# Kernel optimization log

Measured on AMD Instinct MI355X. Metric: run time of the kernel, lower is better.

## Reference

```python
import jax, jax.numpy as jnp
import numpy as np

D_MODEL = 1024
N_HEADS = 16
D_HEAD = D_MODEL // N_HEADS


def setup_inputs() -> dict:
    key = jax.random.key(0)
    ks = jax.random.split(key, 5)
    scale = 1.0 / np.sqrt(D_MODEL)
    return {
        "x": jax.random.normal(ks[0], (2, 2048, D_MODEL), dtype=jnp.float32),
        "W_q": jax.random.normal(ks[1], (D_MODEL, D_MODEL), dtype=jnp.float32) * scale,
        "W_k": jax.random.normal(ks[2], (D_MODEL, D_MODEL), dtype=jnp.float32) * scale,
        "W_v": jax.random.normal(ks[3], (D_MODEL, D_MODEL), dtype=jnp.float32) * scale,
        "W_o": jax.random.normal(ks[4], (D_MODEL, D_MODEL), dtype=jnp.float32) * scale,
    }


def reference(x, W_q, W_k, W_v, W_o):
    B, S, _ = x.shape
    # nn.Linear computes x @ W.T; weights stored [out, in]
    def proj(W):
        y = jnp.einsum("bsd,ed->bse", x, W)
        return y.reshape(B, S, N_HEADS, D_HEAD).transpose(0, 2, 1, 3)  # [B,H,S,Dh]

    q, k, v = proj(W_q), proj(W_k), proj(W_v)
    scores = jnp.einsum("bhqd,bhkd->bhqk", q, k) / jnp.sqrt(jnp.float32(D_HEAD))
    causal = jnp.triu(jnp.ones((S, S), dtype=bool), k=1)
    scores = jnp.where(causal, -jnp.inf, scores)
    attn = jax.nn.softmax(scores, axis=-1)
    out = jnp.einsum("bhqk,bhkd->bhqd", attn, v)  # [B,H,S,Dh]
    out = out.transpose(0, 2, 1, 3).reshape(B, S, D_MODEL)
    return jnp.einsum("bsd,ed->bse", out, W_o)
```

## Files before the change

### kernel.cpp

```cpp
#include <hip/hip_runtime.h>


#define DMODEL 1024
#define NHEADS 16
#define DHEAD  64
#define SEQ    2048
#define BATCH  2
#define MROWS  (BATCH * SEQ)

typedef __bf16 bf16x8 __attribute__((ext_vector_type(8)));
typedef __bf16 bf16x4 __attribute__((ext_vector_type(4)));
typedef float  f32x4  __attribute__((ext_vector_type(4)));

__device__ __forceinline__ f32x4 mfma16(bf16x8 a, bf16x8 b, f32x4 c) {
    return __builtin_amdgcn_mfma_f32_16x16x32_bf16(a, b, c, 0, 0, 0);
}

template <int N>
__device__ __forceinline__ void waitcnt_vm() {
    asm volatile("s_waitcnt vmcnt(%0)" :: "i"(N) : "memory");
}

__device__ __forceinline__ bf16x8 ld8(const float* p) {
    const f32x4 a0 = *(const f32x4*)p;
    const f32x4 a1 = *(const f32x4*)(p + 4);
    bf16x8 v;
    v[0] = (__bf16)a0[0]; v[1] = (__bf16)a0[1];
    v[2] = (__bf16)a0[2]; v[3] = (__bf16)a0[3];
    v[4] = (__bf16)a1[0]; v[5] = (__bf16)a1[1];
    v[6] = (__bf16)a1[2]; v[7] = (__bf16)a1[3];
    return v;
}

__device__ __forceinline__ void gll16(const __bf16* g, __bf16* l) {
    __builtin_amdgcn_global_load_lds(
        (const __attribute__((address_space(1))) void*)g,
        (__attribute__((address_space(3))) void*)l,
        16, 0, 0);
}

__global__ __launch_bounds__(256) void cvt_kernel(const float* __restrict__ x,
                                                  const float* __restrict__ Wq,
                                                  const float* __restrict__ Wk,
                                                  const float* __restrict__ Wv,
                                                  const float* __restrict__ Wo,
                                                  __bf16* __restrict__ xb,
                                                  __bf16* __restrict__ wcat) {
    const int c = blockIdx.x * 256 + threadIdx.x;
    if (c < 524288) {
        *(bf16x8*)(xb + (size_t)c * 8) = ld8(x + (size_t)c * 8);
    } else {
        const int i = c - 524288;
        const int w = i >> 17;
        const int j = i & 131071;
        const float* src = (w == 0) ? Wq : (w == 1) ? Wk : (w == 2) ? Wv : Wo;
        *(bf16x8*)(wcat + (size_t)w * DMODEL * DMODEL + (size_t)j * 8) =
            ld8(src + (size_t)j * 8);
    }
}

template <typename TC, int MREP, int NREP>
__device__ __forceinline__ void gemm_bb_body(const __bf16* __restrict__ A,
                                             const __bf16* __restrict__ W,
                                             TC* __restrict__ C,
                                             __bf16* __restrict__ VT,
                                             bool vt, int m0, int bn0, int cn0,
                                             float scale) {
    constexpr int K  = DMODEL;
    constexpr int TM = MREP * 32;
    constexpr int TN = NREP * 32;
    constexpr int L  = MREP / 2 + NREP / 2;
    __shared__ __align__(16) __bf16 As[3][TM][32];
    __shared__ __align__(16) __bf16 Bs[3][TN][32];

    const int tid  = threadIdx.x;
    const int lane = tid & 63;
    const int wave = tid >> 6;
    const int quad = lane >> 4;
    const int l16  = lane & 15;
    const int wm   = wave & 1;
    const int wn   = wave >> 1;

    const int srow = lane >> 2;
    const int scol = (lane & 3) * 8;

    const __bf16* ap = A + (size_t)(m0 + srow) * K + scol;
    const __bf16* bp = W + (size_t)(bn0 + srow) * K + scol;

    f32x4 acc[MREP][NREP] = {};

    auto stage = [&](int kn, int buf) {
#pragma unroll
        for (int j = 0; j < MREP / 2; ++j) {
            const int r = wave * (MREP * 8) + j * 16;
            gll16(ap + (size_t)r * K + kn, &As[buf][r][0]);
        }
#pragma unroll
        for (int j = 0; j < NREP / 2; ++j) {
            const int r = wave * (NREP * 8) + j * 16;
            gll16(bp + (size_t)r * K + kn, &Bs[buf][r][0]);
        }
    };

    stage(0, 0);
    stage(32, 1);

    int cur = 0;
    for (int k0 = 0; k0 < K; k0 += 32) {
        if (k0 + 64 < K) {
            int b2 = cur + 2; if (b2 >= 3) b2 -= 3;
            stage(k0 + 64, b2);
            waitcnt_vm<2 * L>();
        } else if (k0 + 32 < K) {
            waitcnt_vm<L>();
        } else {
            waitcnt_vm<0>();
        }
        __builtin_amdgcn_s_barrier();
        __builtin_amdgcn_sched_barrier(0);

        bf16x8 af[MREP], bfr[NREP];
#pragma unroll
        for (int i = 0; i < MREP; ++i)
            af[i] = *(const bf16x8*)(&As[cur][wm * (MREP * 16) + i * 16 + l16][quad * 8]);
#pragma unroll
        for (int j = 0; j < NREP; ++j)
            bfr[j] = *(const bf16x8*)(&Bs[cur][wn * (NREP * 16) + j * 16 + l16][quad * 8]);
#pragma unroll
        for (int mi = 0; mi < MREP; ++mi)
#pragma unroll
            for (int ni = 0; ni < NREP; ++ni)
                acc[mi][ni] = mfma16(af[mi], bfr[ni], acc[mi][ni]);

        __builtin_amdgcn_sched_barrier(0);
        __builtin_amdgcn_s_barrier();
        int c1 = cur + 1; if (c1 >= 3) c1 -= 3;
        cur = c1;
    }

    if (!vt) {
#pragma unroll
        for (int mi = 0; mi < MREP; ++mi)
#pragma unroll
            for (int ni = 0; ni < NREP; ++ni)
#pragma unroll
                for (int r = 0; r < 4; ++r) {
                    int row = m0 + wm * (MREP * 16) + mi * 16 + quad * 4 + r;
                    int col = cn0 + wn * (NREP * 16) + ni * 16 + l16;
                    C[(size_t)row * DMODEL + col] = (TC)(acc[mi][ni][r] * scale);
                }
    } else {
#pragma unroll
        for (int mi = 0; mi < MREP; ++mi)
#pragma unroll
            for (int ni = 0; ni < NREP; ++ni) {
                const int m  = m0 + wm * (MREP * 16) + mi * 16 + quad * 4;
                const int hd = cn0 + wn * (NREP * 16) + ni * 16 + l16;
                bf16x4 v4;
#pragma unroll
                for (int r = 0; r < 4; ++r) v4[r] = (__bf16)acc[mi][ni][r];
                *(bf16x4*)(VT + (size_t)hd * MROWS + m) = v4;
            }
    }
}

#define QSCALE 0.1803368801111204f

__global__ __launch_bounds__(256) void qkv_kernel(const __bf16* __restrict__ X,
                                                  const __bf16* __restrict__ wcat,
                                                  __bf16* __restrict__ Q,
                                                  __bf16* __restrict__ K,
                                                  __bf16* __restrict__ VT) {
    const int bn0 = blockIdx.x * 128;
    const int z   = bn0 >> 10;
    const int cn0 = bn0 - (z << 10);
    __bf16* Y = (z == 0) ? Q : K;
    const float scale = (z == 0) ? QSCALE : 1.0f;
    gemm_bb_body<__bf16, 4, 4>(X, wcat, Y, VT, z == 2,
                               blockIdx.y * 128, bn0, cn0, scale);
}

__global__ __launch_bounds__(256) void out_gemm_kernel(const __bf16* __restrict__ A,
                                                       const __bf16* __restrict__ W,
                                                       float* __restrict__ C) {
    gemm_bb_body<float, 2, 4>(A, W, C, nullptr, false,
                              blockIdx.y * 64, blockIdx.x * 128, blockIdx.x * 128,
                              1.0f);
}

__global__ __launch_bounds__(256) void attn_kernel(const __bf16* __restrict__ Q,
                                                   const __bf16* __restrict__ Kg,
                                                   const __bf16* __restrict__ VTg,
                                                   __bf16* __restrict__ O) {
    const int bh  = blockIdx.x;
    const int y   = blockIdx.y;
    const int ya  = y >> 3, yr = y & 7;
    const int qt2 = (ya == 0) ? (31 - yr)
                  : (ya == 1) ? (16 + yr)
                  : (ya == 2) ? (15 - yr)
                  :             yr;
    const int b = bh >> 4, h = bh & 15;
    const size_t base = (size_t)b * SEQ * DMODEL + (size_t)h * DHEAD;

    const int tid  = threadIdx.x;
    const int lane = tid & 63;
    const int wave = tid >> 6;
    const int quad = lane >> 4;
    const int l16  = lane & 15;

    __shared__ __align__(16) __bf16 Ks[2][64][64];
    __shared__ __align__(16) __bf16 Vs[2][64][64];
    __shared__ __align__(16) __bf16 Ps[4][2][16][40];

    const int sr = lane >> 3;
    const int sc = ((lane & 7) ^ sr) * 8;

    const int qrow = qt2 * 64 + wave * 16 + l16;

    const bf16x8 qf0 = *(const bf16x8*)(Q + base + (size_t)qrow * DMODEL + quad * 8);
    const bf16x8 qf1 = *(const bf16x8*)(Q + base + (size_t)qrow * DMODEL + 32 + quad * 8);

    const __bf16* kp = Kg + base + (size_t)(wave * 16 + sr) * DMODEL + sc;
    const __bf16* vp = VTg + (size_t)(h * 64 + wave * 16 + sr) * MROWS
                           + (size_t)b * SEQ + sc;

    bf16x8 ones;
#pragma unroll
    for (int i = 0; i < 8; ++i) ones[i] = (__bf16)1.0f;

    f32x4 oacc[4] = {};
    f32x4 lacc = {};

    const int ntiles = qt2 + 1;
    const int gsw = (l16 & 7);

    gll16(kp, &Ks[0][wave * 16][0]);
    gll16(kp + (size_t)8 * DMODEL, &Ks[0][wave * 16 + 8][0]);
    gll16(vp, &Vs[0][wave * 16][0]);
    gll16(vp + (size_t)8 * MROWS, &Vs[0][wave * 16 + 8][0]);
    __syncthreads();

    int cur = 0;
    for (int kt = 0; kt < ntiles; ++kt) {
        const int k0 = kt * 64;

        if (kt + 1 < ntiles) {
            const __bf16* kpt = kp + (size_t)(k0 + 64) * DMODEL;
            const __bf16* vpt = vp + (k0 + 64);
            gll16(kpt, &Ks[cur ^ 1][wave * 16][0]);
            gll16(kpt + (size_t)8 * DMODEL, &Ks[cur ^ 1][wave * 16 + 8][0]);
            gll16(vpt, &Vs[cur ^ 1][wave * 16][0]);
            gll16(vpt + (size_t)8 * MROWS, &Vs[cur ^ 1][wave * 16 + 8][0]);
        }

        const bool diag = (kt == ntiles - 1);

        f32x4 s[4];
#pragma unroll
        for (int g = 0; g < 4; ++g) {
            const bf16x8 kfa = *(const bf16x8*)(&Ks[cur][g * 16 + l16][(quad ^ gsw) * 8]);
            const bf16x8 kfb = *(const bf16x8*)(&Ks[cur][g * 16 + l16][((quad + 4) ^ gsw) * 8]);
            f32x4 t = {};
            t = mfma16(kfa, qf0, t);
            t = mfma16(kfb, qf1, t);
            s[g] = t;
        }

        bf16x4 w4[4];
        if (!diag) {
#pragma unroll
            for (int g = 0; g < 4; ++g)
#pragma unroll
                for (int r = 0; r < 4; ++r)
                    w4[g][r] = (__bf16)exp2f(s[g][r]);
        } else {
#pragma unroll
            for (int g = 0; g < 4; ++g)
#pragma unroll
                for (int r = 0; r < 4; ++r) {
                    const int kk = k0 + g * 16 + quad * 4 + r;
                    w4[g][r] = (kk <= qrow) ? (__bf16)exp2f(s[g][r]) : (__bf16)0.f;
                }
        }

#pragma unroll
        for (int g = 0; g < 4; ++g)
            *(bf16x4*)(&Ps[wave][g >> 1][l16][(g & 1) * 16 + quad * 4]) = w4[g];

        const bf16x8 pf0 = *(const bf16x8*)(&Ps[wave][0][l16][quad * 8]);
        const bf16x8 pf1 = *(const bf16x8*)(&Ps[wave][1][l16][quad * 8]);
        lacc = mfma16(ones, pf0, lacc);
        lacc = mfma16(ones, pf1, lacc);
#pragma unroll
        for (int f = 0; f < 4; ++f) {
            const bf16x8 vfa = *(const bf16x8*)(&Vs[cur][f * 16 + l16][(quad ^ gsw) * 8]);
            const bf16x8 vfb = *(const bf16x8*)(&Vs[cur][f * 16 + l16][((quad + 4) ^ gsw) * 8]);
            f32x4 t = oacc[f];
            t = mfma16(vfa, pf0, t);
            t = mfma16(vfb, pf1, t);
            oacc[f] = t;
        }

        __syncthreads();
        cur ^= 1;
    }

    const float l_i = lacc[0];
    const float inv = (l_i > 0.f) ? (1.f / l_i) : 0.f;
#pragma unroll
    for (int f = 0; f < 4; ++f) {
        bf16x4 o;
#pragma unroll
        for (int r = 0; r < 4; ++r) o[r] = (__bf16)(oacc[f][r] * inv);
        *(bf16x4*)(O + base + (size_t)qrow * DMODEL + f * 16 + quad * 4) = o;
    }
}

extern "C" void kernel_launch(void* const* d_in, const int* in_sizes, int n_in,
                              void* d_out, int out_size, void* d_ws, size_t ws_size,
                              hipStream_t stream) {
    const float* x  = (const float*)d_in[0];
    const float* Wq = (const float*)d_in[1];
    const float* Wk = (const float*)d_in[2];
    const float* Wv = (const float*)d_in[3];
    const float* Wo = (const float*)d_in[4];
    float* out = (float*)d_out;

    const size_t tm = (size_t)MROWS * DMODEL;
    const size_t tw = (size_t)DMODEL * DMODEL;
    __bf16* Q    = (__bf16*)d_ws;
    __bf16* K    = Q + tm;
    __bf16* VT   = K + tm;
    __bf16* xb   = VT + tm;
    __bf16* wcat = xb + tm;

    cvt_kernel<<<4096, 256, 0, stream>>>(x, Wq, Wk, Wv, Wo, xb, wcat);

    dim3 g1(3072 / 128, MROWS / 128);
    qkv_kernel<<<g1, 256, 0, stream>>>(xb, wcat, Q, K, VT);

    dim3 g2(BATCH * NHEADS, SEQ / 64);
    attn_kernel<<<g2, 256, 0, stream>>>(Q, K, VT, Q);

    dim3 g3(DMODEL / 128, MROWS / 64);
    out_gemm_kernel<<<g3, 256, 0, stream>>>(Q, wcat + 3 * tw, out);
}
```

Before: 177.6 us.

## Process two query tiles per attention block and swap P via permlane

Each attention workgroup now handles 128 query rows (two 64-row tiles A and B) instead of 64. Every K/V tile loaded into shared memory is therefore reused for twice as many queries, which halves K/V global traffic and the number of blocks. The P matrix is also moved from the softmax layout to the MFMA operand layout with v_permlane32/16_swap register shuffles instead of a round trip through shared memory. The cost is higher register pressure from two sets of accumulators, fewer blocks (512 instead of 1024), and wasted masked work on tile A's final diagonal iteration.

```diff
diff --git a/kernel.cpp b/kernel.cpp
--- a/kernel.cpp
+++ b/kernel.cpp
@@ -192,13 +192,9 @@
                                                    const __bf16* __restrict__ Kg,
                                                    const __bf16* __restrict__ VTg,
                                                    __bf16* __restrict__ O) {
-    const int bh  = blockIdx.x;
-    const int y   = blockIdx.y;
-    const int ya  = y >> 3, yr = y & 7;
-    const int qt2 = (ya == 0) ? (31 - yr)
-                  : (ya == 1) ? (16 + yr)
-                  : (ya == 2) ? (15 - yr)
-                  :             yr;
+    const int bh = blockIdx.x;
+    const int y  = blockIdx.y;
+    const int Y  = (y < 8) ? (15 - y) : (y - 8);
     const int b = bh >> 4, h = bh & 15;
     const size_t base = (size_t)b * SEQ * DMODEL + (size_t)h * DHEAD;
 
@@ -210,15 +206,17 @@
 
     __shared__ __align__(16) __bf16 Ks[2][64][64];
     __shared__ __align__(16) __bf16 Vs[2][64][64];
-    __shared__ __align__(16) __bf16 Ps[4][2][16][40];
 
     const int sr = lane >> 3;
     const int sc = ((lane & 7) ^ sr) * 8;
 
-    const int qrow = qt2 * 64 + wave * 16 + l16;
-
-    const bf16x8 qf0 = *(const bf16x8*)(Q + base + (size_t)qrow * DMODEL + quad * 8);
-    const bf16x8 qf1 = *(const bf16x8*)(Q + base + (size_t)qrow * DMODEL + 32 + quad * 8);
+    const int qrowA = Y * 128 + wave * 16 + l16;
+    const int qrowB = qrowA + 64;
+
+    const bf16x8 qfA0 = *(const bf16x8*)(Q + base + (size_t)qrowA * DMODEL + quad * 8);
+    const bf16x8 qfA1 = *(const bf16x8*)(Q + base + (size_t)qrowA * DMODEL + 32 + quad * 8);
+    const bf16x8 qfB0 = *(const bf16x8*)(Q + base + (size_t)qrowB * DMODEL + quad * 8);
+    const bf16x8 qfB1 = *(const bf16x8*)(Q + base + (size_t)qrowB * DMODEL + 32 + quad * 8);
 
     const __bf16* kp = Kg + base + (size_t)(wave * 16 + sr) * DMODEL + sc;
     const __bf16* vp = VTg + (size_t)(h * 64 + wave * 16 + sr) * MROWS
@@ -228,10 +226,10 @@
 #pragma unroll
     for (int i = 0; i < 8; ++i) ones[i] = (__bf16)1.0f;
 
-    f32x4 oacc[4] = {};
-    f32x4 lacc = {};
-
-    const int ntiles = qt2 + 1;
+    f32x4 oaccA[4] = {}, oaccB[4] = {};
+    f32x4 laccA = {}, laccB = {};
+
+    const int ntiles = 2 * Y + 2;
     const int gsw = (l16 & 7);
 
     gll16(kp, &Ks[0][wave * 16][0]);
@@ -253,66 +251,115 @@
             gll16(vpt + (size_t)8 * MROWS, &Vs[cur ^ 1][wave * 16 + 8][0]);
         }
 
-        const bool diag = (kt == ntiles - 1);
-
-        f32x4 s[4];
+        const bool diagA = (kt >= ntiles - 2);
+        const bool diagB = (kt == ntiles - 1);
+
+        f32x4 sA[4], sB[4];
 #pragma unroll
         for (int g = 0; g < 4; ++g) {
             const bf16x8 kfa = *(const bf16x8*)(&Ks[cur][g * 16 + l16][(quad ^ gsw) * 8]);
             const bf16x8 kfb = *(const bf16x8*)(&Ks[cur][g * 16 + l16][((quad + 4) ^ gsw) * 8]);
-            f32x4 t = {};
-            t = mfma16(kfa, qf0, t);
-            t = mfma16(kfb, qf1, t);
-            s[g] = t;
-        }
-
-        bf16x4 w4[4];
-        if (!diag) {
+            f32x4 tA = {};
+            tA = mfma16(kfa, qfA0, tA);
+            tA = mfma16(kfb, qfA1, tA);
+            sA[g] = tA;
+            f32x4 tB = {};
+            tB = mfma16(kfa, qfB0, tB);
+            tB = mfma16(kfb, qfB1, tB);
+            sB[g] = tB;
+        }
+
+        bf16x4 w4A[4], w4B[4];
+        if (!diagA) {
 #pragma unroll
             for (int g = 0; g < 4; ++g)
 #pragma unroll
                 for (int r = 0; r < 4; ++r)
-                    w4[g][r] = (__bf16)exp2f(s[g][r]);
+                    w4A[g][r] = (__bf16)exp2f(sA[g][r]);
         } else {
 #pragma unroll
             for (int g = 0; g < 4; ++g)
 #pragma unroll
                 for (int r = 0; r < 4; ++r) {
                     const int kk = k0 + g * 16 + quad * 4 + r;
-                    w4[g][r] = (kk <= qrow) ? (__bf16)exp2f(s[g][r]) : (__bf16)0.f;
+                    w4A[g][r] = (kk <= qrowA) ? (__bf16)exp2f(sA[g][r]) : (__bf16)0.f;
                 }
         }
-
-#pragma unroll
-        for (int g = 0; g < 4; ++g)
-            *(bf16x4*)(&Ps[wave][g >> 1][l16][(g & 1) * 16 + quad * 4]) = w4[g];
-
-        const bf16x8 pf0 = *(const bf16x8*)(&Ps[wave][0][l16][quad * 8]);
-        const bf16x8 pf1 = *(const bf16x8*)(&Ps[wave][1][l16][quad * 8]);
-        lacc = mfma16(ones, pf0, lacc);
-        lacc = mfma16(ones, pf1, lacc);
+        if (!diagB) {
+#pragma unroll
+            for (int g = 0; g < 4; ++g)
+#pragma unroll
+                for (int r = 0; r < 4; ++r)
+                    w4B[g][r] = (__bf16)exp2f(sB[g][r]);
+        } else {
+#pragma unroll
+            for (int g = 0; g < 4; ++g)
+#pragma unroll
+                for (int r = 0; r < 4; ++r) {
+                    const int kk = k0 + g * 16 + quad * 4 + r;
+                    w4B[g][r] = (kk <= qrowB) ? (__bf16)exp2f(sB[g][r]) : (__bf16)0.f;
+                }
+        }
+
+        unsigned pdA[2][4], pdB[2][4];
+#pragma unroll
+        for (int hh = 0; hh < 2; ++hh)
+#pragma unroll
+            for (int e = 0; e < 2; ++e) {
+                unsigned A0 = ((const unsigned*)&w4A[2 * hh])[e];
+                unsigned B0 = ((const unsigned*)&w4A[2 * hh + 1])[e];
+                asm("v_permlane32_swap_b32 %0, %1" : "+v"(A0), "+v"(B0));
+                asm("v_permlane16_swap_b32 %0, %1" : "+v"(A0), "+v"(B0));
+                pdA[hh][e]     = A0;
+                pdA[hh][2 + e] = B0;
+                unsigned A1 = ((const unsigned*)&w4B[2 * hh])[e];
+                unsigned B1 = ((const unsigned*)&w4B[2 * hh + 1])[e];
+                asm("v_permlane32_swap_b32 %0, %1" : "+v"(A1), "+v"(B1));
+                asm("v_permlane16_swap_b32 %0, %1" : "+v"(A1), "+v"(B1));
+                pdB[hh][e]     = A1;
+                pdB[hh][2 + e] = B1;
+            }
+        const bf16x8 pfA0 = *(const bf16x8*)pdA[0];
+        const bf16x8 pfA1 = *(const bf16x8*)pdA[1];
+        const bf16x8 pfB0 = *(const bf16x8*)pdB[0];
+        const bf16x8 pfB1 = *(const bf16x8*)pdB[1];
+
+        laccA = mfma16(ones, pfA0, laccA);
+        laccA = mfma16(ones, pfA1, laccA);
+        laccB = mfma16(ones, pfB0, laccB);
+        laccB = mfma16(ones, pfB1, laccB);
 #pragma unroll
         for (int f = 0; f < 4; ++f) {
             const bf16x8 vfa = *(const bf16x8*)(&Vs[cur][f * 16 + l16][(quad ^ gsw) * 8]);
             const bf16x8 vfb = *(const bf16x8*)(&Vs[cur][f * 16 + l16][((quad + 4) ^ gsw) * 8]);
-            f32x4 t = oacc[f];
-            t = mfma16(vfa, pf0, t);
-            t = mfma16(vfb, pf1, t);
-            oacc[f] = t;
+            f32x4 tA = oaccA[f];
+            tA = mfma16(vfa, pfA0, tA);
+            tA = mfma16(vfb, pfA1, tA);
+            oaccA[f] = tA;
+            f32x4 tB = oaccB[f];
+            tB = mfma16(vfa, pfB0, tB);
+            tB = mfma16(vfb, pfB1, tB);
+            oaccB[f] = tB;
         }
 
         __syncthreads();
         cur ^= 1;
     }
 
-    const float l_i = lacc[0];
-    const float inv = (l_i > 0.f) ? (1.f / l_i) : 0.f;
+    const float lA = laccA[0];
+    const float invA = (lA > 0.f) ? (1.f / lA) : 0.f;
+    const float lB = laccB[0];
+    const float invB = (lB > 0.f) ? (1.f / lB) : 0.f;
 #pragma unroll
     for (int f = 0; f < 4; ++f) {
-        bf16x4 o;
-#pragma unroll
-        for (int r = 0; r < 4; ++r) o[r] = (__bf16)(oacc[f][r] * inv);
-        *(bf16x4*)(O + base + (size_t)qrow * DMODEL + f * 16 + quad * 4) = o;
+        bf16x4 oA, oB;
+#pragma unroll
+        for (int r = 0; r < 4; ++r) {
+            oA[r] = (__bf16)(oaccA[f][r] * invA);
+            oB[r] = (__bf16)(oaccB[f][r] * invB);
+        }
+        *(bf16x4*)(O + base + (size_t)qrowA * DMODEL + f * 16 + quad * 4) = oA;
+        *(bf16x4*)(O + base + (size_t)qrowB * DMODEL + f * 16 + quad * 4) = oB;
     }
 }
 
@@ -339,7 +386,7 @@
     dim3 g1(3072 / 128, MROWS / 128);
     qkv_kernel<<<g1, 256, 0, stream>>>(xb, wcat, Q, K, VT);
 
-    dim3 g2(BATCH * NHEADS, SEQ / 64);
+    dim3 g2(BATCH * NHEADS, SEQ / 128);
     attn_kernel<<<g2, 256, 0, stream>>>(Q, K, VT, Q);
 
     dim3 g3(DMODEL / 128, MROWS / 64);
```

Result: slower. 194.4 us (+9.5%).
